# Kernel optimization log

Hardware: AMD Instinct MI355X
Metric: run time of the kernel (lower is better)

Reference implementation:

```python
import jax, jax.numpy as jnp
import numpy as np

N, E, D = 50000, 400000, 64
L, NA, NS = 5, 4, 3            # layers, num aggregators, num scalers
ATOM_C, ATOM_V = 9, 64         # OGB-style atom feature columns / vocab
BOND_C, BOND_V = 3, 8
EPS = 1e-5
AVG_LOG = float(np.log(9.0))   # avg_d['log'] = ln(avg_degree + 1), avg_degree = 8


def setup_inputs() -> dict:
    key = jax.random.key(0)
    ks = jax.random.split(key, 8)
    x = jax.random.randint(ks[0], (N, ATOM_C), 0, ATOM_V)
    edge_index = jax.random.randint(ks[1], (2, E), 0, N)
    edge_attr = jax.random.randint(ks[2], (E, BOND_C), 0, BOND_V)
    init = lambda k, shape, fan: (jax.random.normal(k, shape, jnp.float32) / np.sqrt(fan))
    atom_emb = init(ks[3], (ATOM_C, ATOM_V, D), D)
    bond_emb = init(ks[4], (BOND_C, BOND_V, D), D)
    pre_W = init(ks[5], (L, 3 * D, D), 3 * D)                 # pretrans: Linear(3D -> D)
    pre_b = jnp.zeros((L, D), jnp.float32)
    post_W = init(ks[6], (L, (NA * NS + 1) * D, D), (NA * NS + 1) * D)  # posttrans: Linear(13D -> D)
    post_b = jnp.zeros((L, D), jnp.float32)
    return dict(x=x, edge_index=edge_index, edge_attr=edge_attr,
                atom_emb=atom_emb, bond_emb=bond_emb,
                pre_W=pre_W, pre_b=pre_b, post_W=post_W, post_b=post_b)


def reference(x, edge_index, edge_attr, atom_emb, bond_emb, pre_W, pre_b, post_W, post_b):
    src, dst = edge_index[0], edge_index[1]  # PyG: x_j = x[edge_index[0]], x_i = x[edge_index[1]]
    # Encoders: sum of per-column categorical embeddings (OGB Atom/BondEncoder)
    h0 = atom_emb[jnp.arange(ATOM_C)[None, :], x].sum(axis=1)        # [N, D]
    e = bond_emb[jnp.arange(BOND_C)[None, :], edge_attr].sum(axis=1)  # [E, D]
    # message input cat([x_i, x_j, edge_attr]) -- identical for every layer since
    # PNAGNN.forward never feeds layer output back in as x (faithful to source)
    z2 = jnp.concatenate([h0[dst], h0[src], e], axis=-1)              # [E, 3D]
    deg = jax.ops.segment_sum(jnp.ones((E,), jnp.float32), dst, num_segments=N)
    degc = jnp.maximum(deg, 1.0)[:, None]
    log_deg = jnp.log(jnp.maximum(deg, 1.0) + 1.0)[:, None]           # guard deg=0 for attenuation
    amp = log_deg / AVG_LOG
    att = AVG_LOG / log_deg
    has = (deg > 0)[:, None]
    h_in = h0
    for l in range(L):
        m = z2 @ pre_W[l] + pre_b[l]                                  # pretrans (1 layer, no act)
        s_sum = jax.ops.segment_sum(m, dst, num_segments=N)
        mean = s_sum / degc
        mx = jnp.where(has, jax.ops.segment_max(m, dst, num_segments=N), 0.0)
        mn = jnp.where(has, jax.ops.segment_min(m, dst, num_segments=N), 0.0)
        mean_sq = jax.ops.segment_sum(m * m, dst, num_segments=N) / degc
        var = jax.nn.relu(mean_sq - mean * mean)
        std = jnp.sqrt(var + EPS)
        agg = jnp.concatenate([mean, mx, mn, std], axis=-1)           # [N, 4D]
        scaled = jnp.concatenate([agg, agg * amp, agg * att], axis=-1)  # [N, 12D]
        hcat = jnp.concatenate([scaled, h0], axis=-1)                 # [N, 13D]
        out = hcat @ post_W[l] + post_b[l]                            # posttrans (1 layer, no act)
        h = out + h_in                                                # PNAGNN residual
        h_in = h
    return h
```

## Files before the change

### kernel.cpp

```cpp
#include <hip/hip_runtime.h>
#include <hip/hip_bf16.h>

#define NN 50000
#define NE 400000
#define AVG_LOG_F 2.1972245773362196f
#define EPSV 1e-5f

typedef __hip_bfloat16 bf16;
typedef __attribute__((ext_vector_type(8))) short short8v;
typedef __attribute__((ext_vector_type(4))) float f32x4;
typedef __attribute__((ext_vector_type(2))) _Float16 h2v;

__device__ __forceinline__ float b2f(bf16 v){ return __bfloat162float(v); }
__device__ __forceinline__ bf16  f2b(float v){ return __float2bfloat16(v); }
__device__ __forceinline__ short f2s(float v){
  bf16 b = __float2bfloat16(v);
  short s; __builtin_memcpy(&s, &b, 2); return s;
}
__device__ __forceinline__ float s2f(short v){
  bf16 b; __builtin_memcpy(&b, &v, 2); return __bfloat162float(b);
}

__global__ void k_h0(const int* __restrict__ x, const float* __restrict__ aemb,
                     bf16* __restrict__ h0b){
  int idx = blockIdx.x * 256 + threadIdx.x;
  if (idx >= NN * 64) return;
  int n = idx >> 6, d = idx & 63;
  float acc = 0.f;
  #pragma unroll
  for (int c = 0; c < 9; ++c){
    int a = x[n * 9 + c];
    acc += aemb[(c * 64 + a) * 64 + d];
  }
  h0b[idx] = f2b(acc);
}

__global__ void k_deg_code(const int* __restrict__ ei, const int* __restrict__ ea,
                           int* __restrict__ deg, int* __restrict__ code){
  int e = blockIdx.x * 256 + threadIdx.x;
  if (e >= NE) return;
  int dst = ei[NE + e];
  atomicAdd(&deg[dst], 1);
  code[e] = ea[e * 3] + 8 * ea[e * 3 + 1] + 64 * ea[e * 3 + 2];
}

__global__ void k_scan1(const int* __restrict__ deg, int* __restrict__ rowptr,
                        int* __restrict__ part){
  __shared__ int s[256];
  int t = threadIdx.x, i = blockIdx.x * 256 + t;
  int v = (i < NN) ? deg[i] : 0;
  s[t] = v; __syncthreads();
  for (int off = 1; off < 256; off <<= 1){
    int xv = (t >= off) ? s[t - off] : 0;
    __syncthreads();
    s[t] += xv;
    __syncthreads();
  }
  if (i < NN) rowptr[i] = s[t] - v;
  if (t == 255) part[blockIdx.x] = s[255];
}

__global__ void k_scan2(int* __restrict__ part, int nblk){
  __shared__ int s[256];
  int t = threadIdx.x;
  int v = (t < nblk) ? part[t] : 0;
  s[t] = v; __syncthreads();
  for (int off = 1; off < 256; off <<= 1){
    int xv = (t >= off) ? s[t - off] : 0;
    __syncthreads();
    s[t] += xv;
    __syncthreads();
  }
  if (t < nblk) part[t] = s[t] - v;
}

__global__ void k_scan3(int* __restrict__ rowptr, const int* __restrict__ part,
                        const int* __restrict__ deg, float* __restrict__ amp,
                        float* __restrict__ att){
  int i = blockIdx.x * 256 + threadIdx.x;
  if (i < NN){
    rowptr[i] += part[blockIdx.x];
    int d = deg[i];
    float ld = logf((float)max(d, 1) + 1.0f);
    amp[i] = ld / AVG_LOG_F;
    att[i] = AVG_LOG_F / ld;
  }
  if (i == 0) rowptr[NN] = NE;
}

__global__ void k_scatter(const int* __restrict__ ei, const int* __restrict__ code,
                          const int* __restrict__ rowptr, int* __restrict__ cursor,
                          int2* __restrict__ sedge){
  int e = blockIdx.x * 256 + threadIdx.x;
  if (e >= NE) return;
  int dst = ei[NE + e];
  int pos = rowptr[dst] + atomicAdd(&cursor[dst], 1);
  int2 v; v.x = ei[e] * 1664 + 640; v.y = code[e] * 1024;
  sedge[pos] = v;
}

__global__ void k_ctab(const float* __restrict__ bemb, const float* __restrict__ preW,
                       _Float16* __restrict__ CTp){
  __shared__ float et[64];
  int cb = blockIdx.x, l = blockIdx.y, t = threadIdx.x;
  int a0 = cb & 7, a1 = (cb >> 3) & 7, a2 = (cb >> 6) & 7;
  et[t] = bemb[(0 * 8 + a0) * 64 + t] + bemb[(1 * 8 + a1) * 64 + t] + bemb[(2 * 8 + a2) * 64 + t];
  __syncthreads();
  float acc = 0.f;
  const float* W = preW + (l * 192 + 128) * 64;
  for (int k = 0; k < 64; ++k) acc += et[k] * W[k * 64 + t];
  CTp[((size_t)cb * 64 + t) * 8 + l] = (_Float16)acc;
}

__global__ void k_whsum(const float* __restrict__ postW, const float* __restrict__ postb,
                        float* __restrict__ whs, float* __restrict__ bs){
  int idx = blockIdx.x * 256 + threadIdx.x;
  if (idx < 4096){
    int k = idx >> 6, d = idx & 63;
    float a = 0.f;
    for (int l = 0; l < 5; ++l) a += postW[(size_t)(l * 832 + 768 + k) * 64 + d];
    whs[idx] = a;
  }
  if (idx < 64){
    float a = 0.f;
    for (int l = 0; l < 5; ++l) a += postb[l * 64 + idx];
    bs[idx] = a;
  }
}

__global__ void k_wtk(const float* __restrict__ postW, bf16* __restrict__ WtK){
  int idx = blockIdx.x * 256 + threadIdx.x;
  if (idx >= 3 * 64 * 1280) return;
  int g = idx / (64 * 1280);
  int rem = idx % (64 * 1280);
  int c = rem / 1280;
  int kk = rem % 1280;
  int l = kk >> 8, k = kk & 255;
  WtK[idx] = f2b(postW[((size_t)l * 832 + g * 256 + k) * 64 + c]);
}

__global__ void k_wtpre896(const float* __restrict__ preW, const float* __restrict__ preb,
                           const float* __restrict__ whs, const float* __restrict__ bs,
                           bf16* __restrict__ Wtp, float* __restrict__ bias896){
  int idx = blockIdx.x * 256 + threadIdx.x;
  if (idx < 896 * 64){
    int gc = idx >> 6, k = idx & 63;
    float v;
    if (gc < 320){
      int l = gc >> 6, c = gc & 63;
      v = preW[(size_t)(l * 192 + k) * 64 + c];
    } else if (gc < 832){
      int q = gc - 320, d = q >> 3, l = q & 7;
      v = (l < 5) ? preW[(size_t)(l * 192 + 64 + k) * 64 + d] : 0.f;
    } else {
      int c = gc - 832;
      v = whs[k * 64 + c] + ((k == c) ? 1.f : 0.f);
    }
    Wtp[idx] = f2b(v);
  }
  if (idx < 896){
    float b;
    if (idx < 320)      b = preb[(idx >> 6) * 64 + (idx & 63)];
    else if (idx < 832) b = 0.f;
    else                b = bs[idx - 832];
    bias896[idx] = b;
  }
}

__global__ __launch_bounds__(256) void k_ab_mfma(const bf16* __restrict__ h0b,
                                                 const bf16* __restrict__ Wtp,
                                                 const float* __restrict__ bias896,
                                                 _Float16* __restrict__ ABU,
                                                 float* __restrict__ out){
  __shared__ bf16 As[128][72];
  __shared__ bf16 Bs[128][72];
  const int t = threadIdx.x;
  const int n0 = blockIdx.x * 128;
  const int gc0 = blockIdx.y * 128;
  const int lane = t & 63, wid = t >> 6;
  const int rw = wid * 32;
  const short* H  = (const short*)h0b;
  const short* Wp = (const short*)Wtp;

  #pragma unroll
  for (int i = 0; i < 4; ++i){
    int idx = t + i * 256;
    int r = idx >> 3, ko = (idx & 7) * 8;
    int n = n0 + r;
    short8v v = short8v{0,0,0,0,0,0,0,0};
    if (n < NN) v = *(const short8v*)(H + (size_t)n * 64 + ko);
    *(short8v*)&As[r][ko] = v;
  }
  #pragma unroll
  for (int i = 0; i < 4; ++i){
    int idx = t + i * 256;
    int cc = idx >> 3, ko = (idx & 7) * 8;
    *(short8v*)&Bs[cc][ko] = *(const short8v*)(Wp + (size_t)(gc0 + cc) * 64 + ko);
  }
  __syncthreads();

  f32x4 acc[2][8] = {};
  #pragma unroll
  for (int kk = 0; kk < 2; ++kk){
    short8v af0 = *(const short8v*)&As[rw + (lane & 15)][kk * 32 + (lane >> 4) * 8];
    short8v af1 = *(const short8v*)&As[rw + 16 + (lane & 15)][kk * 32 + (lane >> 4) * 8];
    #pragma unroll
    for (int j = 0; j < 8; ++j){
      short8v bfj = *(const short8v*)&Bs[j * 16 + (lane & 15)][kk * 32 + (lane >> 4) * 8];
      acc[0][j] = __builtin_amdgcn_mfma_f32_16x16x32_bf16(af0, bfj, acc[0][j], 0, 0, 0);
      acc[1][j] = __builtin_amdgcn_mfma_f32_16x16x32_bf16(af1, bfj, acc[1][j], 0, 0, 0);
    }
  }

  #pragma unroll
  for (int i = 0; i < 2; ++i){
    #pragma unroll
    for (int r = 0; r < 4; ++r){
      int n = n0 + rw + i * 16 + (lane >> 4) * 4 + r;
      if (n >= NN) continue;
      #pragma unroll
      for (int j = 0; j < 8; ++j){
        int gc = gc0 + j * 16 + (lane & 15);
        float v = acc[i][j][r] + bias896[gc];
        if (gc < 832) ABU[(size_t)n * 832 + gc] = (_Float16)v;
        else          out[(size_t)n * 64 + (gc - 832)] = v;
      }
    }
  }
}

__global__ __launch_bounds__(256) void k_gather(const _Float16* __restrict__ ABU,
                                                const _Float16* __restrict__ CTp,
                                                const int* __restrict__ rowptr,
                                                const int2* __restrict__ sedge,
                                                bf16* __restrict__ AGG){
  const int t = threadIdx.x, lane = t & 63, wid = t >> 6;
  const int n = blockIdx.x * 4 + wid;
  const char* ABUb = (const char*)ABU;
  const char* CTpb = (const char*)CTp;
  short* AGs = (short*)AGG;

  int r0 = rowptr[n], r1 = rowptr[n + 1];
  float s[5]  = {0.f, 0.f, 0.f, 0.f, 0.f};
  float sq[5] = {0.f, 0.f, 0.f, 0.f, 0.f};
  const _Float16 FLO = (_Float16)(-65504.f);
  const _Float16 FHI = (_Float16)( 65504.f);
  h2v mx01 = h2v{FLO, FLO}, mx23 = h2v{FLO, FLO}, mx45 = h2v{FLO, FLO};
  h2v mn01 = h2v{FHI, FHI}, mn23 = h2v{FHI, FHI}, mn45 = h2v{FHI, FHI};

  union P8 { short8v s; h2v h[4]; };
  const int lb = lane * 16;

  for (int j = r0; j < r1; j += 4){
    int rem = r1 - j;
    int2 e0 = sedge[j];
    int2 e1 = (rem > 1) ? sedge[j + 1] : e0;
    int2 e2 = (rem > 2) ? sedge[j + 2] : e0;
    int2 e3 = (rem > 3) ? sedge[j + 3] : e0;
    P8 a0, c0, a1, c1, a2, c2, a3, c3;
    a0.s = *(const short8v*)(ABUb + e0.x + lb);
    c0.s = *(const short8v*)(CTpb + e0.y + lb);
    a1.s = *(const short8v*)(ABUb + e1.x + lb);
    c1.s = *(const short8v*)(CTpb + e1.y + lb);
    a2.s = *(const short8v*)(ABUb + e2.x + lb);
    c2.s = *(const short8v*)(CTpb + e2.y + lb);
    a3.s = *(const short8v*)(ABUb + e3.x + lb);
    c3.s = *(const short8v*)(CTpb + e3.y + lb);

    #define EDGE_ACC(A, C) {                                        \
      h2v t01 = A.h[0] + C.h[0];                                    \
      h2v t23 = A.h[1] + C.h[1];                                    \
      h2v t45 = A.h[2] + C.h[2];                                    \
      mx01 = __builtin_elementwise_max(mx01, t01);                  \
      mx23 = __builtin_elementwise_max(mx23, t23);                  \
      mx45 = __builtin_elementwise_max(mx45, t45);                  \
      mn01 = __builtin_elementwise_min(mn01, t01);                  \
      mn23 = __builtin_elementwise_min(mn23, t23);                  \
      mn45 = __builtin_elementwise_min(mn45, t45);                  \
      float f0 = (float)t01[0], f1 = (float)t01[1];                 \
      float f2 = (float)t23[0], f3 = (float)t23[1];                 \
      float f4 = (float)t45[0];                                     \
      s[0] += f0; sq[0] = fmaf(f0, f0, sq[0]);                      \
      s[1] += f1; sq[1] = fmaf(f1, f1, sq[1]);                      \
      s[2] += f2; sq[2] = fmaf(f2, f2, sq[2]);                      \
      s[3] += f3; sq[3] = fmaf(f3, f3, sq[3]);                      \
      s[4] += f4; sq[4] = fmaf(f4, f4, sq[4]);                      \
    }
    EDGE_ACC(a0, c0);
    if (rem > 1) EDGE_ACC(a1, c1);
    if (rem > 2) EDGE_ACC(a2, c2);
    if (rem > 3) EDGE_ACC(a3, c3);
    #undef EDGE_ACC
  }

  float mx[5] = {(float)mx01[0], (float)mx01[1], (float)mx23[0], (float)mx23[1], (float)mx45[0]};
  float mn[5] = {(float)mn01[0], (float)mn01[1], (float)mn23[0], (float)mn23[1], (float)mn45[0]};

  int d = r1 - r0;
  float degc = (float)((d > 0) ? d : 1);
  size_t base = (size_t)n * 1280;
  #pragma unroll
  for (int l = 0; l < 5; ++l){
    float K = (float)ABU[(size_t)n * 832 + l * 64 + lane];
    float mean = ((float)d * K + s[l]) / degc;
    float MX = (d > 0) ? (K + mx[l]) : 0.f;
    float MN = (d > 0) ? (K + mn[l]) : 0.f;
    float mu = s[l] / degc;
    float var = fmaxf(sq[l] / degc - mu * mu, 0.f);
    float sd = sqrtf(var + EPSV);
    AGs[base + l * 256 + lane]       = f2s(mean);
    AGs[base + l * 256 + 64 + lane]  = f2s(MX);
    AGs[base + l * 256 + 128 + lane] = f2s(MN);
    AGs[base + l * 256 + 192 + lane] = f2s(sd);
  }
}

__global__ __launch_bounds__(512) void k_post5(const bf16* __restrict__ AGG,
                                               const bf16* __restrict__ WtK,
                                               const float* __restrict__ amp,
                                               const float* __restrict__ att,
                                               float* __restrict__ out){
  __shared__ short As[128][140];
  const int t = threadIdx.x, lane = t & 63, wid = t >> 6;
  const int n0 = blockIdx.x * 128;
  const int ks = blockIdx.y;
  const int w4 = wid & 3, rh = wid >> 2;
  const short* AGs = (const short*)AGG;
  const short* Ws  = (const short*)WtK;
  const short8v zv = short8v{0,0,0,0,0,0,0,0};

  f32x4 acc[4][3] = {};
  #pragma unroll
  for (int kt2 = 0; kt2 < 2; ++kt2){
    const int kt = ks * 2 + kt2;
    if (kt2) __syncthreads();
    #pragma unroll
    for (int i = 0; i < 4; ++i){
      int id = t + i * 512;
      int r = id >> 4, ko = (id & 15) * 8;
      int n = n0 + r;
      short8v v = zv;
      if (n < NN) v = *(const short8v*)(AGs + (size_t)n * 1280 + kt * 128 + ko);
      *(short8v*)&As[r][ko] = v;
    }
    __syncthreads();
    #pragma unroll
    for (int kk = 0; kk < 4; ++kk){
      short8v bfg[3];
      #pragma unroll
      for (int g = 0; g < 3; ++g)
        bfg[g] = *(const short8v*)(Ws + (size_t)(g * 64 + w4 * 16 + (lane & 15)) * 1280 +
                                   kt * 128 + kk * 32 + (lane >> 4) * 8);
      #pragma unroll
      for (int rf = 0; rf < 4; ++rf){
        short8v af = *(const short8v*)&As[rh * 64 + rf * 16 + (lane & 15)]
                                         [kk * 32 + (lane >> 4) * 8];
        #pragma unroll
        for (int g = 0; g < 3; ++g)
          acc[rf][g] = __builtin_amdgcn_mfma_f32_16x16x32_bf16(af, bfg[g], acc[rf][g], 0, 0, 0);
      }
    }
  }

  #pragma unroll
  for (int rf = 0; rf < 4; ++rf){
    #pragma unroll
    for (int r = 0; r < 4; ++r){
      int n = n0 + rh * 64 + rf * 16 + (lane >> 4) * 4 + r;
      if (n >= NN) continue;
      float am = amp[n], at = att[n];
      int c = w4 * 16 + (lane & 15);
      float v = acc[rf][0][r] + am * acc[rf][1][r] + at * acc[rf][2][r];
      atomicAdd(&out[(size_t)n * 64 + c], v);
    }
  }
}

extern "C" void kernel_launch(void* const* d_in, const int* in_sizes, int n_in,
                              void* d_out, int out_size, void* d_ws, size_t ws_size,
                              hipStream_t stream){
  const int*   x     = (const int*)d_in[0];
  const int*   ei    = (const int*)d_in[1];
  const int*   ea    = (const int*)d_in[2];
  const float* aemb  = (const float*)d_in[3];
  const float* bemb  = (const float*)d_in[4];
  const float* preW  = (const float*)d_in[5];
  const float* preb  = (const float*)d_in[6];
  const float* postW = (const float*)d_in[7];
  const float* postb = (const float*)d_in[8];
  float* out = (float*)d_out;

  char* p = (char*)d_ws;
  auto alloc = [&](size_t bytes) -> char* {
    char* r = p;
    p += (bytes + 255) & ~(size_t)255;
    return r;
  };
  bf16*      h0b     = (bf16*)     alloc((size_t)NN * 64 * 2);
  _Float16*  ABU     = (_Float16*) alloc((size_t)NN * 832 * 2);
  bf16*      AGG     = (bf16*)     alloc((size_t)NN * 1280 * 2);
  int*       deg     = (int*)      alloc((size_t)NN * 4);
  int*       rowptr  = (int*)      alloc((size_t)(NN + 1) * 4);
  int*       cursor  = (int*)      alloc((size_t)NN * 4);
  float*     amp     = (float*)    alloc((size_t)NN * 4);
  float*     att     = (float*)    alloc((size_t)NN * 4);
  int*       code    = (int*)      alloc((size_t)NE * 4);
  int2*      sedge   = (int2*)     alloc((size_t)NE * 8);
  _Float16*  CTp     = (_Float16*) alloc((size_t)512 * 64 * 8 * 2 + 64);
  float*     whs     = (float*)    alloc((size_t)64 * 64 * 4);
  float*     bs      = (float*)    alloc((size_t)64 * 4);
  int*       part    = (int*)      alloc((size_t)256 * 4);
  bf16*      WtK     = (bf16*)     alloc((size_t)3 * 64 * 1280 * 2);
  bf16*      Wtp     = (bf16*)     alloc((size_t)896 * 64 * 2);
  float*     bias896 = (float*)    alloc((size_t)896 * 4);
  if ((size_t)(p - (char*)d_ws) > ws_size) return;

  hipMemsetAsync(deg, 0, (size_t)NN * 4, stream);
  hipMemsetAsync(cursor, 0, (size_t)NN * 4, stream);

  k_h0<<<dim3((NN * 64 + 255) / 256), 256, 0, stream>>>(x, aemb, h0b);
  k_deg_code<<<dim3((NE + 255) / 256), 256, 0, stream>>>(ei, ea, deg, code);
  int nblk = (NN + 255) / 256;
  k_scan1<<<dim3(nblk), 256, 0, stream>>>(deg, rowptr, part);
  k_scan2<<<dim3(1), 256, 0, stream>>>(part, nblk);
  k_scan3<<<dim3(nblk), 256, 0, stream>>>(rowptr, part, deg, amp, att);
  k_scatter<<<dim3((NE + 255) / 256), 256, 0, stream>>>(ei, code, rowptr, cursor, sedge);
  k_ctab<<<dim3(512, 5), 64, 0, stream>>>(bemb, preW, CTp);
  k_whsum<<<dim3(16), 256, 0, stream>>>(postW, postb, whs, bs);
  k_wtk<<<dim3((3 * 64 * 1280 + 255) / 256), 256, 0, stream>>>(postW, WtK);
  k_wtpre896<<<dim3((896 * 64 + 255) / 256), 256, 0, stream>>>(preW, preb, whs, bs,
                                                               Wtp, bias896);
  k_ab_mfma<<<dim3((NN + 127) / 128, 7), 256, 0, stream>>>(h0b, Wtp, bias896, ABU, out);
  k_gather<<<dim3(NN / 4), 256, 0, stream>>>(ABU, CTp, rowptr, sedge, AGG);
  k_post5<<<dim3((NN + 127) / 128, 5), 512, 0, stream>>>(AGG, WtK, amp, att, out);
}
```

Before: 309.2 us.

## Store aggregates and post weights in MFMA fragment order, drop LDS and atomics

The gather kernel now writes aggregated features straight into a tiled layout that matches the MFMA 16x16x32 operand fragments. The post-transform weights are pre-permuted into the same fragment order. k_post5 then streams A and B fragments directly from global memory with no LDS staging or barriers, and covers the full K=1280 per block. Because the K dimension is no longer split across blocks, the output update becomes a plain read-modify-write instead of atomicAdd. The trade-off is less parallelism per output tile, and gather now does scattered 2-byte stores into the tiled buffer.

```diff
diff --git a/kernel.cpp b/kernel.cpp
--- a/kernel.cpp
+++ b/kernel.cpp
@@ -128,15 +128,19 @@
   }
 }
 
-__global__ void k_wtk(const float* __restrict__ postW, bf16* __restrict__ WtK){
+__global__ void k_wtk(const float* __restrict__ postW, bf16* __restrict__ WtKf){
   int idx = blockIdx.x * 256 + threadIdx.x;
-  if (idx >= 3 * 64 * 1280) return;
-  int g = idx / (64 * 1280);
-  int rem = idx % (64 * 1280);
-  int c = rem / 1280;
-  int kk = rem % 1280;
-  int l = kk >> 8, k = kk & 255;
-  WtK[idx] = f2b(postW[((size_t)l * 832 + g * 256 + k) * 64 + c]);
+  if (idx >= 40 * 12 * 64 * 8) return;
+  int s   = idx / 6144;
+  int rem = idx % 6144;
+  int gw  = rem / 512;
+  int lane = (rem % 512) / 8;
+  int j   = idx & 7;
+  int g = gw >> 2, w4 = gw & 3;
+  int kp = s * 32 + (lane >> 4) * 8 + j;
+  int l = kp >> 8, kl = kp & 255;
+  int c = w4 * 16 + (lane & 15);
+  WtKf[idx] = f2b(postW[((size_t)l * 832 + g * 256 + kl) * 64 + c]);
 }
 
 __global__ void k_wtpre896(const float* __restrict__ preW, const float* __restrict__ preb,
@@ -233,12 +237,11 @@
                                                 const _Float16* __restrict__ CTp,
                                                 const int* __restrict__ rowptr,
                                                 const int2* __restrict__ sedge,
-                                                bf16* __restrict__ AGG){
+                                                bf16* __restrict__ AGGf){
   const int t = threadIdx.x, lane = t & 63, wid = t >> 6;
   const int n = blockIdx.x * 4 + wid;
   const char* ABUb = (const char*)ABU;
   const char* CTpb = (const char*)CTp;
-  short* AGs = (short*)AGG;
 
   int r0 = rowptr[n], r1 = rowptr[n + 1];
   float s[5]  = {0.f, 0.f, 0.f, 0.f, 0.f};
@@ -298,7 +301,8 @@
 
   int d = r1 - r0;
   float degc = (float)((d > 0) ? d : 1);
-  size_t base = (size_t)n * 1280;
+  const int loff = ((lane >> 5) << 10) + (((lane & 31) >> 3) << 8) + ((lane & 7) << 1);
+  char* basep = (char*)AGGf + (size_t)(n >> 4) * 40960 + (n & 15) * 16 + loff;
   #pragma unroll
   for (int l = 0; l < 5; ++l){
     float K = (float)ABU[(size_t)n * 832 + l * 64 + lane];
@@ -308,70 +312,50 @@
     float mu = s[l] / degc;
     float var = fmaxf(sq[l] / degc - mu * mu, 0.f);
     float sd = sqrtf(var + EPSV);
-    AGs[base + l * 256 + lane]       = f2s(mean);
-    AGs[base + l * 256 + 64 + lane]  = f2s(MX);
-    AGs[base + l * 256 + 128 + lane] = f2s(MN);
-    AGs[base + l * 256 + 192 + lane] = f2s(sd);
-  }
-}
-
-__global__ __launch_bounds__(512) void k_post5(const bf16* __restrict__ AGG,
-                                               const bf16* __restrict__ WtK,
+    char* pl = basep + l * 8192;
+    *(short*)(pl)        = f2s(mean);
+    *(short*)(pl + 2048) = f2s(MX);
+    *(short*)(pl + 4096) = f2s(MN);
+    *(short*)(pl + 6144) = f2s(sd);
+  }
+}
+
+__global__ __launch_bounds__(256) void k_post5(const bf16* __restrict__ AGGf,
+                                               const bf16* __restrict__ WtKf,
                                                const float* __restrict__ amp,
                                                const float* __restrict__ att,
                                                float* __restrict__ out){
-  __shared__ short As[128][140];
-  const int t = threadIdx.x, lane = t & 63, wid = t >> 6;
-  const int n0 = blockIdx.x * 128;
-  const int ks = blockIdx.y;
-  const int w4 = wid & 3, rh = wid >> 2;
-  const short* AGs = (const short*)AGG;
-  const short* Ws  = (const short*)WtK;
-  const short8v zv = short8v{0,0,0,0,0,0,0,0};
-
-  f32x4 acc[4][3] = {};
-  #pragma unroll
-  for (int kt2 = 0; kt2 < 2; ++kt2){
-    const int kt = ks * 2 + kt2;
-    if (kt2) __syncthreads();
-    #pragma unroll
-    for (int i = 0; i < 4; ++i){
-      int id = t + i * 512;
-      int r = id >> 4, ko = (id & 15) * 8;
-      int n = n0 + r;
-      short8v v = zv;
-      if (n < NN) v = *(const short8v*)(AGs + (size_t)n * 1280 + kt * 128 + ko);
-      *(short8v*)&As[r][ko] = v;
-    }
-    __syncthreads();
-    #pragma unroll
-    for (int kk = 0; kk < 4; ++kk){
-      short8v bfg[3];
-      #pragma unroll
-      for (int g = 0; g < 3; ++g)
-        bfg[g] = *(const short8v*)(Ws + (size_t)(g * 64 + w4 * 16 + (lane & 15)) * 1280 +
-                                   kt * 128 + kk * 32 + (lane >> 4) * 8);
-      #pragma unroll
-      for (int rf = 0; rf < 4; ++rf){
-        short8v af = *(const short8v*)&As[rh * 64 + rf * 16 + (lane & 15)]
-                                         [kk * 32 + (lane >> 4) * 8];
-        #pragma unroll
-        for (int g = 0; g < 3; ++g)
-          acc[rf][g] = __builtin_amdgcn_mfma_f32_16x16x32_bf16(af, bfg[g], acc[rf][g], 0, 0, 0);
-      }
-    }
-  }
-
-  #pragma unroll
-  for (int rf = 0; rf < 4; ++rf){
+  const int t = threadIdx.x, lane = t & 63, w4 = t >> 6;
+  const int rg0 = blockIdx.x * 2;
+  const char* pa0 = (const char*)AGGf + (size_t)rg0 * 40960 + lane * 16;
+  const char* pa1 = pa0 + 40960;
+  const char* pb  = (const char*)WtKf + w4 * 1024 + lane * 16;
+
+  f32x4 acc[2][3] = {};
+  for (int s = 0; s < 40; ++s){
+    short8v a0 = *(const short8v*)(pa0);
+    short8v a1 = *(const short8v*)(pa1);
+    short8v b0 = *(const short8v*)(pb);
+    short8v b1 = *(const short8v*)(pb + 4096);
+    short8v b2 = *(const short8v*)(pb + 8192);
+    acc[0][0] = __builtin_amdgcn_mfma_f32_16x16x32_bf16(a0, b0, acc[0][0], 0, 0, 0);
+    acc[0][1] = __builtin_amdgcn_mfma_f32_16x16x32_bf16(a0, b1, acc[0][1], 0, 0, 0);
+    acc[0][2] = __builtin_amdgcn_mfma_f32_16x16x32_bf16(a0, b2, acc[0][2], 0, 0, 0);
+    acc[1][0] = __builtin_amdgcn_mfma_f32_16x16x32_bf16(a1, b0, acc[1][0], 0, 0, 0);
+    acc[1][1] = __builtin_amdgcn_mfma_f32_16x16x32_bf16(a1, b1, acc[1][1], 0, 0, 0);
+    acc[1][2] = __builtin_amdgcn_mfma_f32_16x16x32_bf16(a1, b2, acc[1][2], 0, 0, 0);
+    pa0 += 1024; pa1 += 1024; pb += 12288;
+  }
+
+  #pragma unroll
+  for (int i = 0; i < 2; ++i){
     #pragma unroll
     for (int r = 0; r < 4; ++r){
-      int n = n0 + rh * 64 + rf * 16 + (lane >> 4) * 4 + r;
+      int n = (rg0 + i) * 16 + (lane >> 4) * 4 + r;
       if (n >= NN) continue;
       float am = amp[n], at = att[n];
       int c = w4 * 16 + (lane & 15);
-      float v = acc[rf][0][r] + am * acc[rf][1][r] + at * acc[rf][2][r];
-      atomicAdd(&out[(size_t)n * 64 + c], v);
+      out[(size_t)n * 64 + c] += acc[i][0][r] + am * acc[i][1][r] + at * acc[i][2][r];
     }
   }
 }
@@ -398,7 +382,7 @@
   };
   bf16*      h0b     = (bf16*)     alloc((size_t)NN * 64 * 2);
   _Float16*  ABU     = (_Float16*) alloc((size_t)NN * 832 * 2);
-  bf16*      AGG     = (bf16*)     alloc((size_t)NN * 1280 * 2);
+  bf16*      AGGf    = (bf16*)     alloc((size_t)3126 * 40960);
   int*       deg     = (int*)      alloc((size_t)NN * 4);
   int*       rowptr  = (int*)      alloc((size_t)(NN + 1) * 4);
   int*       cursor  = (int*)      alloc((size_t)NN * 4);
@@ -410,7 +394,7 @@
   float*     whs     = (float*)    alloc((size_t)64 * 64 * 4);
   float*     bs      = (float*)    alloc((size_t)64 * 4);
   int*       part    = (int*)      alloc((size_t)256 * 4);
-  bf16*      WtK     = (bf16*)     alloc((size_t)3 * 64 * 1280 * 2);
+  bf16*      WtKf    = (bf16*)     alloc((size_t)40 * 12 * 64 * 8 * 2);
   bf16*      Wtp     = (bf16*)     alloc((size_t)896 * 64 * 2);
   float*     bias896 = (float*)    alloc((size_t)896 * 4);
   if ((size_t)(p - (char*)d_ws) > ws_size) return;
@@ -427,10 +411,10 @@
   k_scatter<<<dim3((NE + 255) / 256), 256, 0, stream>>>(ei, code, rowptr, cursor, sedge);
   k_ctab<<<dim3(512, 5), 64, 0, stream>>>(bemb, preW, CTp);
   k_whsum<<<dim3(16), 256, 0, stream>>>(postW, postb, whs, bs);
-  k_wtk<<<dim3((3 * 64 * 1280 + 255) / 256), 256, 0, stream>>>(postW, WtK);
+  k_wtk<<<dim3((40 * 12 * 64 * 8 + 255) / 256), 256, 0, stream>>>(postW, WtKf);
   k_wtpre896<<<dim3((896 * 64 + 255) / 256), 256, 0, stream>>>(preW, preb, whs, bs,
                                                                Wtp, bias896);
   k_ab_mfma<<<dim3((NN + 127) / 128, 7), 256, 0, stream>>>(h0b, Wtp, bias896, ABU, out);
-  k_gather<<<dim3(NN / 4), 256, 0, stream>>>(ABU, CTp, rowptr, sedge, AGG);
-  k_post5<<<dim3((NN + 127) / 128, 5), 512, 0, stream>>>(AGG, WtK, amp, att, out);
-}
+  k_gather<<<dim3(NN / 4), 256, 0, stream>>>(ABU, CTp, rowptr, sedge, AGGf);
+  k_post5<<<dim3((3125 + 1) / 2), 256, 0, stream>>>(AGGf, WtKf, amp, att, out);
+}
```

Measured after the change: 314.4 us. About the same (+1.7%).
